# Kernel optimization log

Hardware: AMD Instinct MI355X
Metric: run time of the kernel (lower is better)

## Reference

```python
import jax, jax.numpy as jnp
import numpy as np

B = 256          # batch size
D = 512          # feature_size
P = 5            # num_parts
NC = 11003       # num_classes
SEGC = 6         # segmentation classes
H = 64           # mask spatial size
SCALE = 28.0
ALPHA, BETA = 0.6, 0.4
SP, SN = 10.0, 40.0
TOPK = 8


def _l2n(x, axis):
    return x / jnp.linalg.norm(x, axis=axis, keepdims=True)


def setup_inputs() -> dict:
    key = jax.random.key(0)
    ks = jax.random.split(key, 10)
    return {
        "visual_embed": jax.random.normal(ks[0], (B, D), jnp.float32),
        "textual_embed": jax.random.normal(ks[1], (B, D), jnp.float32),
        "part_embed": jax.random.normal(ks[2], (P, B, D), jnp.float32),
        "attribute_embed": jax.random.normal(ks[3], (P, B, D), jnp.float32),
        "seg_feat": jax.random.normal(ks[4], (B * P, SEGC, H, H), jnp.float32),
        "W": jax.random.normal(ks[5], (D, NC), jnp.float32),
        "labels": jax.random.randint(ks[6], (B,), 0, NC, jnp.int64) if jax.config.jax_enable_x64 else jax.random.randint(ks[6], (B,), 0, NC, jnp.int32),
        "masks": jax.random.randint(ks[7], (B * P, H, H), 0, SEGC, jnp.int32),
        "vmask": jax.random.randint(ks[8], (B, P), 0, 2).astype(bool),
        "tmask": jax.random.randint(ks[9], (B, P), 0, 2).astype(bool),
    }


def _instance_loss(visual_embed, textual_embed, W, labels):
    vn = _l2n(visual_embed, 1)
    tn = _l2n(textual_embed, 1)
    Wn = _l2n(W, 0)
    v_logits = SCALE * (vn @ Wn)          # [B, NC]
    t_logits = SCALE * (tn @ Wn)
    idx = jnp.arange(labels.shape[0])
    v_loss = -jax.nn.log_softmax(v_logits, axis=-1)[idx, labels].mean()
    t_loss = -jax.nn.log_softmax(t_logits, axis=-1)[idx, labels].mean()
    return v_loss + t_loss


def _mask_loss(seg_feat, masks):
    logp = jax.nn.log_softmax(seg_feat, axis=1)                      # [BP, C, H, H]
    ce = -jnp.take_along_axis(logp, masks[:, None, :, :], axis=1)[:, 0]
    return P * ce.mean()


def _global_align_loss(visual_embed, textual_embed, labels):
    vn = _l2n(visual_embed, 1)
    tn = _l2n(textual_embed, 1)
    sim = vn @ tn.T                                                  # [B, B]
    match = labels[:, None] == labels[None, :]
    Lp = jax.nn.softplus(-SP * (sim - ALPHA))
    Ln = jax.nn.softplus(SN * (sim - BETA))
    # original loops over rows then columns, each covering the full matrix
    return 2.0 * jnp.where(match, Lp, Ln).sum() / labels.shape[0]


def _local_align_loss(part_embed, attribute_embed, labels, vmask, tmask):
    pe = _l2n(part_embed, 2)
    ae = _l2n(attribute_embed, 2)
    match = labels[:, None] == labels[None, :]
    bsz = labels.shape[0]
    total = jnp.float32(0.0)
    for i in range(P):  # small fixed loop over parts
        pm = vmask[:, i]
        am = tmask[:, i]
        sim = pe[i] @ ae[i].T                                        # [B, B]
        r1 = jnp.argsort(-sim, axis=1)
        r2 = jnp.argsort(-sim.T, axis=1)
        # NOTE: original code indexes rank1/rank2 with the PART index i
        # (not the sample index j), so the pseudo-label boost is constant
        # across samples within a part; reproduced faithfully.
        fwd1 = r1[i, :TOPK]
        hit1 = (r2[fwd1, :TOPK] == i).any(axis=1)
        boost1 = jnp.zeros(bsz, bool).at[fwd1].set(hit1)
        fwd2 = r2[i, :TOPK]
        hit2 = (r1[fwd2, :TOPK] == i).any(axis=1)
        boost2 = jnp.zeros(bsz, bool).at[fwd2].set(hit2)
        Lp = jax.nn.softplus(-SP * (sim - ALPHA))
        Ln = jax.nn.softplus(SN * (sim - BETA))
        # branch 1: rows j with pm[j], columns k with am[k]
        pos1 = match | boost1[None, :]
        w1 = (pm[:, None] & am[None, :]).astype(sim.dtype)
        b1 = (jnp.where(pos1, Lp, Ln) * w1).sum()
        # branch 2: samples j with pm[j]&am[j], rows k with pm[k]; pred = sim[k, j]
        pos2 = match | boost2[None, :]
        w2 = ((pm & am)[:, None] & pm[None, :]).astype(sim.dtype)
        b2 = (jnp.where(pos2, Lp.T, Ln.T) * w2).sum()
        total = total + (b1 + b2) / bsz
    return total / P


def reference(visual_embed, textual_embed, part_embed, attribute_embed, seg_feat, W,
              labels, masks, vmask, tmask):
    instance_loss = _instance_loss(visual_embed, textual_embed, W, labels)
    mask_loss = _mask_loss(seg_feat, masks)
    global_align_loss = _global_align_loss(visual_embed, textual_embed, labels)
    local_align_loss = _local_align_loss(part_embed, attribute_embed, labels, vmask, tmask)
    return (instance_loss, mask_loss, global_align_loss, local_align_loss)
```

## Files before the change

### kernel.cpp

```cpp
#include <hip/hip_runtime.h>
#include <stdint.h>
#include <stddef.h>

#define BB 256
#define DD 512
#define PP 5
#define NCLS 11003
#define NCP 11008
#define SEGC 6
#define SCALEF 28.0f
#define ALPHAF 0.6f
#define BETAF 0.4f
#define SPF 10.0f
#define SNF 40.0f

typedef __attribute__((ext_vector_type(8))) short bf16x8;
typedef __attribute__((ext_vector_type(4))) float f32x4;

__device__ __forceinline__ float waveSum(float v) {
#pragma unroll
    for (int o = 32; o; o >>= 1) v += __shfl_down(v, o);
    return v;
}

__device__ __forceinline__ float softplusf(float x) {
    return fmaxf(x, 0.f) + log1pf(__expf(-fabsf(x)));
}

__device__ __forceinline__ short to_bf16(float f) {
    uint32_t u = __float_as_uint(f);
    uint32_t r = (u + 0x7FFFu + ((u >> 16) & 1u)) >> 16;
    return (short)r;
}

__global__ __launch_bounds__(256) void convert_k(const void* labels_raw,
                                                 const void* vm_raw,
                                                 const void* tm_raw,
                                                 int* __restrict__ labs,
                                                 unsigned char* __restrict__ vmb,
                                                 unsigned char* __restrict__ tmb) {
    __shared__ int is64, v32, t32;
    if (threadIdx.x == 0) {
        const int* L = (const int*)labels_raw;
        int f = 1;
        for (int j = 0; j < 16; j++) if (L[2 * j + 1] != 0) f = 0;
        is64 = f;
        const int* V = (const int*)vm_raw;
        f = 1;
        for (int j = 0; j < 16; j++) if ((unsigned)V[j] > 1u) f = 0;
        v32 = f;
        const int* T = (const int*)tm_raw;
        f = 1;
        for (int j = 0; j < 16; j++) if ((unsigned)T[j] > 1u) f = 0;
        t32 = f;
    }
    __syncthreads();
    int i = threadIdx.x;
    if (i < BB) {
        if (is64) labs[i] = (int)((const long long*)labels_raw)[i];
        else      labs[i] = ((const int*)labels_raw)[i];
    }
    for (int j = i; j < BB * PP; j += 256) {
        vmb[j] = v32 ? (unsigned char)(((const int*)vm_raw)[j] != 0)
                     : (unsigned char)(((const unsigned char*)vm_raw)[j] != 0);
        tmb[j] = t32 ? (unsigned char)(((const int*)tm_raw)[j] != 0)
                     : (unsigned char)(((const unsigned char*)tm_raw)[j] != 0);
    }
}

__global__ __launch_bounds__(256) void norm_rows_k(const float* __restrict__ src,
                                                   float* __restrict__ dst,
                                                   short* __restrict__ dstb) {
    int row = blockIdx.x;
    const float* s = src + (size_t)row * DD;
    float v0 = s[threadIdx.x];
    float v1 = s[threadIdx.x + 256];
    float ss = v0 * v0 + v1 * v1;
    __shared__ float red[4];
    __shared__ float inv;
    float v = waveSum(ss);
    if ((threadIdx.x & 63) == 0) red[threadIdx.x >> 6] = v;
    __syncthreads();
    if (threadIdx.x == 0) inv = 1.0f / sqrtf(red[0] + red[1] + red[2] + red[3]);
    __syncthreads();
    float a = v0 * inv, b = v1 * inv;
    float* d = dst + (size_t)row * DD;
    d[threadIdx.x] = a;
    d[threadIdx.x + 256] = b;
    if (dstb) {
        short* db = dstb + (size_t)row * DD;
        db[threadIdx.x] = to_bf16(a);
        db[threadIdx.x + 256] = to_bf16(b);
    }
}

__global__ __launch_bounds__(128) void wsq_k(const float* __restrict__ W,
                                             float* __restrict__ swn_sq) {
    int c = blockIdx.x * 128 + threadIdx.x;
    if (c >= NCLS) return;
    int k0 = blockIdx.y * 64;
    float ss = 0.f;
    for (int k = k0; k < k0 + 64; k++) {
        float w = W[(size_t)k * NCLS + c];
        ss = fmaf(w, w, ss);
    }
    atomicAdd(&swn_sq[c], ss);
}

__global__ __launch_bounds__(256) void wfin_k(const float* __restrict__ swn_sq,
                                              float* __restrict__ swn) {
    int c = blockIdx.x * 256 + threadIdx.x;
    if (c < NCLS) swn[c] = SCALEF / sqrtf(swn_sq[c]);
}

__global__ __launch_bounds__(256) void wtrans_k(const float* __restrict__ W,
                                                short* __restrict__ Wt) {
    __shared__ short tile[32][66];
    int c0 = blockIdx.x * 64, k0 = blockIdx.y * 32;
    int t = threadIdx.x;
    int cl = t & 63, kl = t >> 6;
#pragma unroll
    for (int it = 0; it < 8; it++) {
        int k = k0 + kl + it * 4;
        int c = c0 + cl;
        float w = (c < NCLS) ? W[(size_t)k * NCLS + c] : 0.f;
        tile[kl + it * 4][cl] = to_bf16(w);
    }
    __syncthreads();
    int c_l = t >> 2, kc = (t & 3) * 8;
    bf16x8 v;
#pragma unroll
    for (int i = 0; i < 8; i++) v[i] = tile[kc + i][c_l];
    *(bf16x8*)(Wt + (size_t)(c0 + c_l) * DD + k0 + kc) = v;
}

__global__ __launch_bounds__(256) void logits_mfma_k(const short* __restrict__ Xb,
                                                     const short* __restrict__ Wt,
                                                     const float* __restrict__ swn,
                                                     float* __restrict__ sumexp) {
    int wave = threadIdx.x >> 6;
    int lane = threadIdx.x & 63;
    int l15 = lane & 15, lh = lane >> 4;
    int row0 = blockIdx.y * 64 + wave * 16;
    int col0 = blockIdx.x * 64;
    f32x4 acc0 = {0.f, 0.f, 0.f, 0.f};
    f32x4 acc1 = acc0, acc2 = acc0, acc3 = acc0;
    const short* ap = Xb + (size_t)(row0 + l15) * DD + lh * 8;
    const short* bp = Wt + (size_t)(col0 + l15) * DD + lh * 8;
#pragma unroll
    for (int kb = 0; kb < DD; kb += 32) {
        bf16x8 a = *(const bf16x8*)(ap + kb);
        bf16x8 b0 = *(const bf16x8*)(bp + kb);
        bf16x8 b1 = *(const bf16x8*)(bp + 16 * DD + kb);
        bf16x8 b2 = *(const bf16x8*)(bp + 32 * DD + kb);
        bf16x8 b3 = *(const bf16x8*)(bp + 48 * DD + kb);
        acc0 = __builtin_amdgcn_mfma_f32_16x16x32_bf16(a, b0, acc0, 0, 0, 0);
        acc1 = __builtin_amdgcn_mfma_f32_16x16x32_bf16(a, b1, acc1, 0, 0, 0);
        acc2 = __builtin_amdgcn_mfma_f32_16x16x32_bf16(a, b2, acc2, 0, 0, 0);
        acc3 = __builtin_amdgcn_mfma_f32_16x16x32_bf16(a, b3, acc3, 0, 0, 0);
    }
    float s0 = 0.f, s1 = 0.f, s2 = 0.f, s3 = 0.f;
#pragma unroll
    for (int j = 0; j < 4; j++) {
        int c = col0 + 16 * j + l15;
        bool valid = c < NCLS;
        float sc = valid ? swn[c] : 0.f;
        f32x4 accj = (j == 0) ? acc0 : (j == 1) ? acc1 : (j == 2) ? acc2 : acc3;
        s0 += valid ? __expf(accj[0] * sc) : 0.f;
        s1 += valid ? __expf(accj[1] * sc) : 0.f;
        s2 += valid ? __expf(accj[2] * sc) : 0.f;
        s3 += valid ? __expf(accj[3] * sc) : 0.f;
    }
#pragma unroll
    for (int o = 1; o < 16; o <<= 1) {
        s0 += __shfl_xor(s0, o);
        s1 += __shfl_xor(s1, o);
        s2 += __shfl_xor(s2, o);
        s3 += __shfl_xor(s3, o);
    }
    if (l15 == 0) {
        int rbase = row0 + 4 * lh;
        atomicAdd(&sumexp[rbase + 0], s0);
        atomicAdd(&sumexp[rbase + 1], s1);
        atomicAdd(&sumexp[rbase + 2], s2);
        atomicAdd(&sumexp[rbase + 3], s3);
    }
}

__global__ __launch_bounds__(256) void inst_label_k(const float* __restrict__ Xn,
                                                    const float* __restrict__ W,
                                                    const float* __restrict__ swn,
                                                    const float* __restrict__ sumexp,
                                                    const int* __restrict__ labs,
                                                    double* __restrict__ iacc) {
    int i = blockIdx.x;
    int t = threadIdx.x;
    int lab = labs[i];
    float dv = 0.f, dt_ = 0.f;
    for (int k = t; k < DD; k += 256) {
        float w = W[(size_t)k * NCLS + lab];
        dv = fmaf(Xn[(size_t)i * DD + k], w, dv);
        dt_ = fmaf(Xn[(size_t)(BB + i) * DD + k], w, dt_);
    }
    __shared__ float rv[4], rt[4];
    float a = waveSum(dv), b = waveSum(dt_);
    if ((t & 63) == 0) { rv[t >> 6] = a; rt[t >> 6] = b; }
    __syncthreads();
    if (t == 0) {
        float sc = swn[lab];
        float dvs = (rv[0] + rv[1] + rv[2] + rv[3]) * sc;
        float dts = (rt[0] + rt[1] + rt[2] + rt[3]) * sc;
        float li = (logf(sumexp[i]) - dvs) + (logf(sumexp[BB + i]) - dts);
        atomicAdd(iacc, (double)li);
    }
}

__global__ __launch_bounds__(256) void mask_loss_k(const float* __restrict__ seg,
                                                   const int* __restrict__ masks,
                                                   double* __restrict__ acc) {
    int idx = blockIdx.x * 256 + threadIdx.x;
    int n = idx >> 12;
    int pix = idx & 4095;
    const float* p = seg + (size_t)n * SEGC * 4096 + pix;
    float x0 = p[0], x1 = p[4096], x2 = p[8192];
    float x3 = p[12288], x4 = p[16384], x5 = p[20480];
    float mx = fmaxf(fmaxf(fmaxf(x0, x1), fmaxf(x2, x3)), fmaxf(x4, x5));
    float se = __expf(x0 - mx) + __expf(x1 - mx) + __expf(x2 - mx) +
               __expf(x3 - mx) + __expf(x4 - mx) + __expf(x5 - mx);
    int m = masks[idx];
    float xm = (m == 0) ? x0 : (m == 1) ? x1 : (m == 2) ? x2
             : (m == 3) ? x3 : (m == 4) ? x4 : x5;
    float ce = logf(se) + mx - xm;
    __shared__ float red[4];
    float v = waveSum(ce);
    if ((threadIdx.x & 63) == 0) red[threadIdx.x >> 6] = v;
    __syncthreads();
    if (threadIdx.x == 0)
        atomicAdd(&acc[blockIdx.x & 63], (double)(red[0] + red[1] + red[2] + red[3]));
}

__global__ __launch_bounds__(256) void sim_k(const float* __restrict__ vn,
                                             const float* __restrict__ tn,
                                             const float* __restrict__ pn,
                                             const float* __restrict__ an,
                                             float* __restrict__ sims) {
    int z = blockIdx.z;
    const float* X;
    const float* Y;
    if (z == 0) { X = vn; Y = tn; }
    else { X = pn + (size_t)(z - 1) * BB * DD; Y = an + (size_t)(z - 1) * BB * DD; }
    float* C = sims + (size_t)z * BB * BB;
    int row0 = blockIdx.y * 32, col0 = blockIdx.x * 32;
    int tx = threadIdx.x & 15, ty = threadIdx.x >> 4;
    __shared__ float Xs[32][33], Ys[32][33];
    float a00 = 0, a01 = 0, a10 = 0, a11 = 0;
    for (int kc = 0; kc < DD; kc += 32) {
#pragma unroll
        for (int l = 0; l < 4; l++) {
            int idx = threadIdx.x + l * 256;
            int r = idx >> 5, kk = idx & 31;
            Xs[r][kk] = X[(size_t)(row0 + r) * DD + kc + kk];
            Ys[r][kk] = Y[(size_t)(col0 + r) * DD + kc + kk];
        }
        __syncthreads();
#pragma unroll
        for (int kk = 0; kk < 32; kk++) {
            float x0 = Xs[ty * 2][kk], x1 = Xs[ty * 2 + 1][kk];
            float y0 = Ys[tx * 2][kk], y1 = Ys[tx * 2 + 1][kk];
            a00 = fmaf(x0, y0, a00);
            a01 = fmaf(x0, y1, a01);
            a10 = fmaf(x1, y0, a10);
            a11 = fmaf(x1, y1, a11);
        }
        __syncthreads();
    }
    int r = row0 + ty * 2, c = col0 + tx * 2;
    C[(size_t)r * BB + c] = a00;
    C[(size_t)r * BB + c + 1] = a01;
    C[(size_t)(r + 1) * BB + c] = a10;
    C[(size_t)(r + 1) * BB + c + 1] = a11;
}

__global__ __launch_bounds__(256) void boost_k(const float* __restrict__ sims,
                                               unsigned char* __restrict__ b1,
                                               unsigned char* __restrict__ b2) {
    int i = blockIdx.x;
    const float* S = sims + (size_t)(i + 1) * BB * BB;
    int c = threadIdx.x;
    __shared__ float rowv[BB], colv[BB];
    rowv[c] = S[(size_t)i * BB + c];
    colv[c] = S[(size_t)c * BB + i];
    __syncthreads();
    float rv = rowv[c], cv = colv[c];
    int rank1 = 0, rank2 = 0;
    for (int j = 0; j < BB; j++) {
        rank1 += rowv[j] > rv;
        rank2 += colv[j] > cv;
    }
    unsigned char bo1 = 0, bo2 = 0;
    if (rank1 < 8) {
        int cnt = 0;
        for (int a = 0; a < BB; a++) cnt += S[(size_t)a * BB + c] > rv;
        bo1 = (cnt < 8);
    }
    if (rank2 < 8) {
        int cnt = 0;
        for (int b = 0; b < BB; b++) cnt += S[(size_t)c * BB + b] > cv;
        bo2 = (cnt < 8);
    }
    b1[i * BB + c] = bo1;
    b2[i * BB + c] = bo2;
}

__global__ __launch_bounds__(256) void galign_k(const float* __restrict__ sim,
                                                const int* __restrict__ labs,
                                                double* __restrict__ acc) {
    int r = blockIdx.x, c = threadIdx.x;
    float s = sim[(size_t)r * BB + c];
    float x = (labs[r] == labs[c]) ? (-SPF * (s - ALPHAF)) : (SNF * (s - BETAF));
    float v = softplusf(x);
    __shared__ float red[4];
    v = waveSum(v);
    if ((threadIdx.x & 63) == 0) red[threadIdx.x >> 6] = v;
    __syncthreads();
    if (threadIdx.x == 0)
        atomicAdd(&acc[blockIdx.x & 7], (double)(red[0] + red[1] + red[2] + red[3]));
}

__global__ __launch_bounds__(256) void lalign_k(const float* __restrict__ sims,
                                                const int* __restrict__ labs,
                                                const unsigned char* __restrict__ vmb,
                                                const unsigned char* __restrict__ tmb,
                                                const unsigned char* __restrict__ b1,
                                                const unsigned char* __restrict__ b2,
                                                double* __restrict__ acc) {
    int i = blockIdx.y, r = blockIdx.x, c = threadIdx.x;
    const float* S = sims + (size_t)(i + 1) * BB * BB;
    float s = S[(size_t)r * BB + c];
    bool m = labs[r] == labs[c];
    float Lp = softplusf(-SPF * (s - ALPHAF));
    float Ln = softplusf(SNF * (s - BETAF));
    bool pmr = vmb[r * PP + i] != 0;
    bool pmc = vmb[c * PP + i] != 0;
    bool amc = tmb[c * PP + i] != 0;
    float v = 0.f;
    if (pmr && amc) v += (m || (b1[i * BB + c] != 0)) ? Lp : Ln;
    if (pmc && amc && pmr) v += (m || (b2[i * BB + r] != 0)) ? Lp : Ln;
    __shared__ float red[4];
    v = waveSum(v);
    if ((threadIdx.x & 63) == 0) red[threadIdx.x >> 6] = v;
    __syncthreads();
    if (threadIdx.x == 0)
        atomicAdd(&acc[blockIdx.x & 7], (double)(red[0] + red[1] + red[2] + red[3]));
}

__global__ void finalize_k(const double* __restrict__ accs, float* __restrict__ out) {
    int t = threadIdx.x;
    double mv = accs[t];
    double gv = (t < 8) ? accs[64 + t] : 0.0;
    double lv = (t < 8) ? accs[72 + t] : 0.0;
#pragma unroll
    for (int o = 32; o; o >>= 1) {
        mv += __shfl_down(mv, o);
        gv += __shfl_down(gv, o);
        lv += __shfl_down(lv, o);
    }
    if (t == 0) {
        out[0] = (float)(accs[80] / (double)BB);
        out[1] = (float)((double)PP * mv / 5242880.0);
        out[2] = (float)(2.0 * gv / (double)BB);
        out[3] = (float)(lv / (double)(BB * PP));
    }
}

extern "C" void kernel_launch(void* const* d_in, const int* in_sizes, int n_in,
                              void* d_out, int out_size, void* d_ws, size_t ws_size,
                              hipStream_t stream) {
    const float* visual  = (const float*)d_in[0];
    const float* textual = (const float*)d_in[1];
    const float* part    = (const float*)d_in[2];
    const float* attr    = (const float*)d_in[3];
    const float* seg     = (const float*)d_in[4];
    const float* W       = (const float*)d_in[5];
    const void*  labels  = d_in[6];
    const int*   masks   = (const int*)d_in[7];
    const void*  vmask   = d_in[8];
    const void*  tmask   = d_in[9];
    float* out = (float*)d_out;

    float* ws = (float*)d_ws;
    short* Wt   = (short*)ws;
    float* base = ws + (size_t)NCP * DD / 2;
    short* Xb   = (short*)base;
    float* vn   = base + (size_t)BB * DD;
    float* tn   = vn + (size_t)BB * DD;
    float* pn   = tn + (size_t)BB * DD;
    float* an   = pn + (size_t)PP * BB * DD;
    float* swn  = an + (size_t)PP * BB * DD;
    float* swn_sq = swn + NCP;
    float* sims = swn_sq + NCP;
    float* sumexp = sims + 6 * BB * BB;
    int* labs = (int*)(sumexp + 2 * BB);
    unsigned char* vmb = (unsigned char*)(labs + BB);
    unsigned char* tmb = vmb + BB * PP;
    unsigned char* b1  = tmb + BB * PP;
    unsigned char* b2  = b1 + BB * PP;
    uintptr_t aaddr = ((uintptr_t)(b2 + BB * PP) + 15) & ~(uintptr_t)15;
    double* accs = (double*)aaddr;

    hipMemsetAsync(sumexp, 0, 2 * BB * sizeof(float), stream);
    hipMemsetAsync(swn_sq, 0, NCP * sizeof(float), stream);
    hipMemsetAsync(accs, 0, 81 * sizeof(double), stream);

    convert_k<<<1, 256, 0, stream>>>(labels, vmask, tmask, labs, vmb, tmb);

    norm_rows_k<<<BB, 256, 0, stream>>>(visual, vn, Xb);
    norm_rows_k<<<BB, 256, 0, stream>>>(textual, tn, Xb + (size_t)BB * DD);
    norm_rows_k<<<PP * BB, 256, 0, stream>>>(part, pn, nullptr);
    norm_rows_k<<<PP * BB, 256, 0, stream>>>(attr, an, nullptr);

    dim3 wg(86, 8);
    wsq_k<<<wg, 128, 0, stream>>>(W, swn_sq);
    wfin_k<<<NCP / 256, 256, 0, stream>>>(swn_sq, swn);
    dim3 tg(NCP / 64, 16);
    wtrans_k<<<tg, 256, 0, stream>>>(W, Wt);

    dim3 mg(NCP / 64, 8);
    logits_mfma_k<<<mg, 256, 0, stream>>>(Xb, Wt, swn, sumexp);
    inst_label_k<<<BB, 256, 0, stream>>>(vn, W, swn, sumexp, labs, accs + 80);

    mask_loss_k<<<5242880 / 256, 256, 0, stream>>>(seg, masks, accs);

    dim3 sg(8, 8, 6);
    sim_k<<<sg, 256, 0, stream>>>(vn, tn, pn, an, sims);
    boost_k<<<PP, 256, 0, stream>>>(sims, b1, b2);

    galign_k<<<BB, 256, 0, stream>>>(sims, labs, accs + 64);
    dim3 lg(BB, PP);
    lalign_k<<<lg, 256, 0, stream>>>(sims, labs, vmb, tmb, b1, b2, accs + 72);

    finalize_k<<<1, 64, 0, stream>>>(accs, out);
}
```

Before: 426.0 us.

## Pre-swizzle bf16 operands into MFMA fragment layout and fold W-norm finalize

The normalized embeddings and the transposed W are now written directly in the per-lane MFMA fragment order, so each lane's bf16x8 load in the logits kernel is contiguous across the wave. This replaces strided row loads of 1 KB rows with coalesced 1 KB chunks per k-tile. The separate wfin_k launch is removed, and the scale factor is computed inline from swn_sq in the consumers. The cost is extra sqrt/div work in the epilogues and more complex index math in the producer kernels.

```diff
diff --git a/kernel.cpp b/kernel.cpp
--- a/kernel.cpp
+++ b/kernel.cpp
@@ -70,7 +70,8 @@
 
 __global__ __launch_bounds__(256) void norm_rows_k(const float* __restrict__ src,
                                                    float* __restrict__ dst,
-                                                   short* __restrict__ dstb) {
+                                                   short* __restrict__ Xp,
+                                                   int row_base) {
     int row = blockIdx.x;
     const float* s = src + (size_t)row * DD;
     float v0 = s[threadIdx.x];
@@ -87,10 +88,19 @@
     float* d = dst + (size_t)row * DD;
     d[threadIdx.x] = a;
     d[threadIdx.x + 256] = b;
-    if (dstb) {
-        short* db = dstb + (size_t)row * DD;
-        db[threadIdx.x] = to_bf16(a);
-        db[threadIdx.x + 256] = to_bf16(b);
+    if (Xp) {
+        int prow = row_base + row;
+        int rt = prow >> 4, rl = prow & 15;
+#pragma unroll
+        for (int h = 0; h < 2; h++) {
+            int c = threadIdx.x + h * 256;
+            float val = h ? b : a;
+            int kt = c >> 5;
+            int lh = (c & 31) >> 3;
+            int i = c & 7;
+            int lane = (lh << 4) | rl;
+            Xp[((size_t)(rt * 16 + kt) * 64 + lane) * 8 + i] = to_bf16(val);
+        }
     }
 }
 
@@ -107,53 +117,49 @@
     atomicAdd(&swn_sq[c], ss);
 }
 
-__global__ __launch_bounds__(256) void wfin_k(const float* __restrict__ swn_sq,
-                                              float* __restrict__ swn) {
-    int c = blockIdx.x * 256 + threadIdx.x;
-    if (c < NCLS) swn[c] = SCALEF / sqrtf(swn_sq[c]);
-}
-
 __global__ __launch_bounds__(256) void wtrans_k(const float* __restrict__ W,
-                                                short* __restrict__ Wt) {
+                                                short* __restrict__ Wp) {
     __shared__ short tile[32][66];
     int c0 = blockIdx.x * 64, k0 = blockIdx.y * 32;
     int t = threadIdx.x;
-    int cl = t & 63, kl = t >> 6;
+    int cl64 = t & 63, kl = t >> 6;
 #pragma unroll
     for (int it = 0; it < 8; it++) {
         int k = k0 + kl + it * 4;
-        int c = c0 + cl;
+        int c = c0 + cl64;
         float w = (c < NCLS) ? W[(size_t)k * NCLS + c] : 0.f;
-        tile[kl + it * 4][cl] = to_bf16(w);
-    }
-    __syncthreads();
-    int c_l = t >> 2, kc = (t & 3) * 8;
+        tile[kl + it * 4][cl64] = to_bf16(w);
+    }
+    __syncthreads();
+    int ctl = t >> 6, lane = t & 63;
+    int cl = lane & 15, lh = lane >> 4;
     bf16x8 v;
 #pragma unroll
-    for (int i = 0; i < 8; i++) v[i] = tile[kc + i][c_l];
-    *(bf16x8*)(Wt + (size_t)(c0 + c_l) * DD + k0 + kc) = v;
-}
-
-__global__ __launch_bounds__(256) void logits_mfma_k(const short* __restrict__ Xb,
-                                                     const short* __restrict__ Wt,
-                                                     const float* __restrict__ swn,
+    for (int i = 0; i < 8; i++) v[i] = tile[lh * 8 + i][ctl * 16 + cl];
+    int ct = blockIdx.x * 4 + ctl;
+    *(bf16x8*)(Wp + ((size_t)(ct * 16 + blockIdx.y) * 64 + lane) * 8) = v;
+}
+
+__global__ __launch_bounds__(256) void logits_mfma_k(const short* __restrict__ Xp,
+                                                     const short* __restrict__ Wp,
+                                                     const float* __restrict__ swn_sq,
                                                      float* __restrict__ sumexp) {
     int wave = threadIdx.x >> 6;
     int lane = threadIdx.x & 63;
     int l15 = lane & 15, lh = lane >> 4;
-    int row0 = blockIdx.y * 64 + wave * 16;
-    int col0 = blockIdx.x * 64;
+    int rt = blockIdx.y * 4 + wave;
+    int ct0 = blockIdx.x * 4;
     f32x4 acc0 = {0.f, 0.f, 0.f, 0.f};
     f32x4 acc1 = acc0, acc2 = acc0, acc3 = acc0;
-    const short* ap = Xb + (size_t)(row0 + l15) * DD + lh * 8;
-    const short* bp = Wt + (size_t)(col0 + l15) * DD + lh * 8;
-#pragma unroll
-    for (int kb = 0; kb < DD; kb += 32) {
-        bf16x8 a = *(const bf16x8*)(ap + kb);
-        bf16x8 b0 = *(const bf16x8*)(bp + kb);
-        bf16x8 b1 = *(const bf16x8*)(bp + 16 * DD + kb);
-        bf16x8 b2 = *(const bf16x8*)(bp + 32 * DD + kb);
-        bf16x8 b3 = *(const bf16x8*)(bp + 48 * DD + kb);
+    const short* ap = Xp + (size_t)rt * 16 * 64 * 8 + lane * 8;
+    const short* bp = Wp + (size_t)ct0 * 16 * 64 * 8 + lane * 8;
+#pragma unroll
+    for (int kt = 0; kt < 16; kt++) {
+        bf16x8 a  = *(const bf16x8*)(ap + (size_t)kt * 512);
+        bf16x8 b0 = *(const bf16x8*)(bp + (size_t)kt * 512);
+        bf16x8 b1 = *(const bf16x8*)(bp + (size_t)(16 * 512) + kt * 512);
+        bf16x8 b2 = *(const bf16x8*)(bp + (size_t)(32 * 512) + kt * 512);
+        bf16x8 b3 = *(const bf16x8*)(bp + (size_t)(48 * 512) + kt * 512);
         acc0 = __builtin_amdgcn_mfma_f32_16x16x32_bf16(a, b0, acc0, 0, 0, 0);
         acc1 = __builtin_amdgcn_mfma_f32_16x16x32_bf16(a, b1, acc1, 0, 0, 0);
         acc2 = __builtin_amdgcn_mfma_f32_16x16x32_bf16(a, b2, acc2, 0, 0, 0);
@@ -162,9 +168,9 @@
     float s0 = 0.f, s1 = 0.f, s2 = 0.f, s3 = 0.f;
 #pragma unroll
     for (int j = 0; j < 4; j++) {
-        int c = col0 + 16 * j + l15;
+        int c = (ct0 + j) * 16 + l15;
         bool valid = c < NCLS;
-        float sc = valid ? swn[c] : 0.f;
+        float sc = valid ? SCALEF / sqrtf(swn_sq[c]) : 0.f;
         f32x4 accj = (j == 0) ? acc0 : (j == 1) ? acc1 : (j == 2) ? acc2 : acc3;
         s0 += valid ? __expf(accj[0] * sc) : 0.f;
         s1 += valid ? __expf(accj[1] * sc) : 0.f;
@@ -179,7 +185,7 @@
         s3 += __shfl_xor(s3, o);
     }
     if (l15 == 0) {
-        int rbase = row0 + 4 * lh;
+        int rbase = rt * 16 + 4 * lh;
         atomicAdd(&sumexp[rbase + 0], s0);
         atomicAdd(&sumexp[rbase + 1], s1);
         atomicAdd(&sumexp[rbase + 2], s2);
@@ -189,7 +195,7 @@
 
 __global__ __launch_bounds__(256) void inst_label_k(const float* __restrict__ Xn,
                                                     const float* __restrict__ W,
-                                                    const float* __restrict__ swn,
+                                                    const float* __restrict__ swn_sq,
                                                     const float* __restrict__ sumexp,
                                                     const int* __restrict__ labs,
                                                     double* __restrict__ iacc) {
@@ -207,7 +213,7 @@
     if ((t & 63) == 0) { rv[t >> 6] = a; rt[t >> 6] = b; }
     __syncthreads();
     if (t == 0) {
-        float sc = swn[lab];
+        float sc = SCALEF / sqrtf(swn_sq[lab]);
         float dvs = (rv[0] + rv[1] + rv[2] + rv[3]) * sc;
         float dts = (rt[0] + rt[1] + rt[2] + rt[3]) * sc;
         float li = (logf(sumexp[i]) - dvs) + (logf(sumexp[BB + i]) - dts);
@@ -389,15 +395,14 @@
     float* out = (float*)d_out;
 
     float* ws = (float*)d_ws;
-    short* Wt   = (short*)ws;
+    short* Wp   = (short*)ws;
     float* base = ws + (size_t)NCP * DD / 2;
-    short* Xb   = (short*)base;
+    short* Xp   = (short*)base;
     float* vn   = base + (size_t)BB * DD;
     float* tn   = vn + (size_t)BB * DD;
     float* pn   = tn + (size_t)BB * DD;
     float* an   = pn + (size_t)PP * BB * DD;
-    float* swn  = an + (size_t)PP * BB * DD;
-    float* swn_sq = swn + NCP;
+    float* swn_sq = an + (size_t)PP * BB * DD;
     float* sims = swn_sq + NCP;
     float* sumexp = sims + 6 * BB * BB;
     int* labs = (int*)(sumexp + 2 * BB);
@@ -414,20 +419,19 @@
 
     convert_k<<<1, 256, 0, stream>>>(labels, vmask, tmask, labs, vmb, tmb);
 
-    norm_rows_k<<<BB, 256, 0, stream>>>(visual, vn, Xb);
-    norm_rows_k<<<BB, 256, 0, stream>>>(textual, tn, Xb + (size_t)BB * DD);
-    norm_rows_k<<<PP * BB, 256, 0, stream>>>(part, pn, nullptr);
-    norm_rows_k<<<PP * BB, 256, 0, stream>>>(attr, an, nullptr);
+    norm_rows_k<<<BB, 256, 0, stream>>>(visual, vn, Xp, 0);
+    norm_rows_k<<<BB, 256, 0, stream>>>(textual, tn, Xp, BB);
+    norm_rows_k<<<PP * BB, 256, 0, stream>>>(part, pn, nullptr, 0);
+    norm_rows_k<<<PP * BB, 256, 0, stream>>>(attr, an, nullptr, 0);
 
     dim3 wg(86, 8);
     wsq_k<<<wg, 128, 0, stream>>>(W, swn_sq);
-    wfin_k<<<NCP / 256, 256, 0, stream>>>(swn_sq, swn);
     dim3 tg(NCP / 64, 16);
-    wtrans_k<<<tg, 256, 0, stream>>>(W, Wt);
+    wtrans_k<<<tg, 256, 0, stream>>>(W, Wp);
 
     dim3 mg(NCP / 64, 8);
-    logits_mfma_k<<<mg, 256, 0, stream>>>(Xb, Wt, swn, sumexp);
-    inst_label_k<<<BB, 256, 0, stream>>>(vn, W, swn, sumexp, labs, accs + 80);
+    logits_mfma_k<<<mg, 256, 0, stream>>>(Xp, Wp, swn_sq, sumexp);
+    inst_label_k<<<BB, 256, 0, stream>>>(vn, W, swn_sq, sumexp, labs, accs + 80);
 
     mask_loss_k<<<5242880 / 256, 256, 0, stream>>>(seg, masks, accs);
 
```

Result: faster. 386.7 us (-9.2%).
